# Kernel optimization log

Hardware: AMD Instinct MI355X
Metric: run time of the kernel (lower is better)

The kernel has to match this reference:

```python
import jax, jax.numpy as jnp
import numpy as np
from jax.scipy.linalg import solve_triangular

N, S, G, D = 2048, 64, 1, 512


def setup_inputs() -> dict:
    key = jax.random.key(0)
    k1, k2, k3, k4 = jax.random.split(key, 4)
    x = jax.random.normal(k1, (N, D), jnp.float32)
    mu = jax.random.uniform(k2, (S, G, D), jnp.float32) - 0.5  # torch.rand(...) - 0.5
    omega = jax.random.normal(k3, (S, G), jnp.float32)
    # original init sets sigma_p = eye; perturb so m = A^T A has distinct eigenvalues
    sigma_p = jnp.eye(D, dtype=jnp.float32)[None, None] + 0.05 * jax.random.normal(k4, (S, G, D, D), jnp.float32)
    return {"x": x, "mu": mu, "omega": omega, "sigma_p": sigma_p}


def reference(x, mu, omega, sigma_p):
    d = x.shape[-1]
    # m = sigma_p^T @ sigma_p  (symmetric PSD), per class/component
    m = jnp.einsum('sgki,sgkj->sgij', sigma_p, sigma_p)  # (S,G,D,D)
    # torch: sigma = m + 0.01 * diag_embed(eig(m).eigenvalues.real) * eye(d)
    # m is symmetric PSD -> eigenvalues are real; eigvalsh is the batched symmetric form
    eigvals = jnp.linalg.eigvalsh(m)  # (S,G,D)
    sigma = m + 0.01 * eigvals[..., None] * jnp.eye(d, dtype=m.dtype)  # adds diag(eigvals)
    _ = jax.nn.softmax(omega, -1)  # computed in original forward but unused in output
    mu0 = mu[:, 0]        # (S,D)   only component 0 is used
    sig0 = sigma[:, 0]    # (S,D,D)
    # MultivariateNormal.log_prob via Cholesky, batched over classes and samples
    L = jnp.linalg.cholesky(sig0)               # (S,D,D)
    diff = x[None, :, :] - mu0[:, None, :]      # (S,N,D)
    z = solve_triangular(L, diff.swapaxes(-1, -2), lower=True)  # (S,D,N)
    maha = jnp.sum(z * z, axis=1)               # (S,N)
    logdet = 2.0 * jnp.sum(jnp.log(jnp.diagonal(L, axis1=-2, axis2=-1)), axis=-1)  # (S,)
    logp = -0.5 * (maha + logdet[:, None] + d * jnp.log(jnp.asarray(2.0 * np.pi, m.dtype)))
    return logp.T  # (N,S)
```

## Files before the change

kernel.cpp:

```cpp
#include <hip/hip_runtime.h>

#define D 512
#define TW 16

__device__ __forceinline__ float waveSum(float v) {
#pragma unroll
    for (int m = 32; m > 0; m >>= 1) v += __shfl_xor(v, m, 64);
    return v;
}
__device__ __forceinline__ float waveMin(float v) {
#pragma unroll
    for (int m = 32; m > 0; m >>= 1) v = fminf(v, __shfl_xor(v, m, 64));
    return v;
}
__device__ __forceinline__ float waveMax(float v) {
#pragma unroll
    for (int m = 32; m > 0; m >>= 1) v = fmaxf(v, __shfl_xor(v, m, 64));
    return v;
}

__global__ __launch_bounds__(256) void xpose_kernel(const float* __restrict__ x,
                                                    float* __restrict__ xT) {
    __shared__ float t[64][65];
    const int bx = blockIdx.x * 64;
    const int by = blockIdx.y * 64;
    const int tid = threadIdx.x;
    const int lx = tid & 63, lq = tid >> 6;
#pragma unroll
    for (int r = 0; r < 64; r += 4)
        t[r + lq][lx] = x[(size_t)(bx + r + lq) * D + by + lx];
    __syncthreads();
#pragma unroll
    for (int r = 0; r < 64; r += 4)
        xT[(size_t)(by + r + lq) * 2048 + bx + lx] = t[lx][r + lq];
}

__global__ __launch_bounds__(256) void syrk_kernel(const float* __restrict__ sp,
                                                   float* __restrict__ M) {
    const int s = blockIdx.y;
    const int I = blockIdx.x >> 3, J = blockIdx.x & 7;
    const int tx = threadIdx.x & 15, ty = threadIdx.x >> 4;
    const float* __restrict__ A = sp + (size_t)s * D * D;
    __shared__ __align__(16) float As[64 * 68];
    __shared__ __align__(16) float Bs[64 * 68];
    float acc[4][4];
#pragma unroll
    for (int r = 0; r < 4; r++)
#pragma unroll
        for (int q = 0; q < 4; q++) acc[r][q] = 0.f;

    for (int k0 = 0; k0 < D; k0 += 64) {
        for (int e = threadIdx.x; e < 4096; e += 256) {
            const int col = e & 63, kr = e >> 6;
            As[kr * 68 + col] = A[(size_t)(k0 + kr) * D + I * 64 + col];
            Bs[kr * 68 + col] = A[(size_t)(k0 + kr) * D + J * 64 + col];
        }
        __syncthreads();
#pragma unroll 4
        for (int k = 0; k < 64; k++) {
            const float4 a = *(const float4*)&As[k * 68 + 4 * ty];
            const float4 b = *(const float4*)&Bs[k * 68 + 4 * tx];
            const float av[4] = {a.x, a.y, a.z, a.w};
            const float bv[4] = {b.x, b.y, b.z, b.w};
#pragma unroll
            for (int r = 0; r < 4; r++)
#pragma unroll
                for (int q = 0; q < 4; q++) acc[r][q] += av[r] * bv[q];
        }
        __syncthreads();
    }
#pragma unroll
    for (int r = 0; r < 4; r++) {
        float4 v4;
        v4.x = acc[r][0]; v4.y = acc[r][1]; v4.z = acc[r][2]; v4.w = acc[r][3];
        const size_t off = (size_t)s * D * D + (size_t)(I * 64 + 4 * ty + r) * D + J * 64 + 4 * tx;
        *(float4*)(M + off) = v4;
    }
}

__global__ __launch_bounds__(1024) void latrd_panel(float* __restrict__ T,
                                                    float* __restrict__ Vt,
                                                    float* __restrict__ Wt,
                                                    float* __restrict__ dvec,
                                                    float* __restrict__ evec,
                                                    int ps, int jmax) {
    const int s = blockIdx.x;
    float* __restrict__ Ts = T + (size_t)s * D * D;
    float* __restrict__ Vg = Vt + (size_t)s * 32 * D;
    float* __restrict__ Wg = Wt + (size_t)s * 32 * D;
    const int tid = threadIdx.x, lane = tid & 63, wid = tid >> 6;
    const int l4 = lane & 15, quad = lane >> 4;
    extern __shared__ float sm[];
    float* __restrict__ Vs = sm;
    float* __restrict__ Ws = sm + 16896;
    float* __restrict__ vb = sm + 33792;
    float* __restrict__ pf = sm + 34304;
    float* __restrict__ c1 = sm + 34816;
    float* __restrict__ c2 = sm + 34848;
    float* __restrict__ red = sm + 34880;
    float* __restrict__ sca = sm + 34896;

    for (int i = tid; i < 34304; i += 1024) sm[i] = 0.f;
    __syncthreads();

    float rk = (tid < D) ? Ts[(size_t)ps * D + tid] : 0.f;

    for (int j = 0; j < jmax; j++) {
        const int k = ps + j, sup = k + 1;
        float val = 0.f;
        if (tid < D && tid > k) {
            float corr = 0.f;
#pragma unroll 4
            for (int t = 0; t < j; t++)
                corr += Vs[tid * 33 + t] * Ws[k * 33 + t]
                      + Ws[tid * 33 + t] * Vs[k * 33 + t];
            val = rk - corr;
            vb[tid] = val;
            if (tid == sup) sca[3] = val;
        } else if (tid == k) {
            float dc = 0.f;
            for (int t = 0; t < j; t++) dc += Vs[k * 33 + t] * Ws[k * 33 + t];
            dvec[s * D + k] = rk - 2.f * dc;
            vb[k] = 0.f;
        }
        float xp = (tid < D && tid > sup) ? val * val : 0.f;
        xp = waveSum(xp);
        if (lane == 0) red[wid] = xp;
        __syncthreads();

        float xn2 = 0.f;
#pragma unroll
        for (int q = 0; q < TW; q++) xn2 += red[q];
        const float a0 = sca[3];
        const int skip = (xn2 <= 0.f);
        float beta = 0.f, v0 = 0.f, alpha = a0;
        if (!skip) {
            const float an = sqrtf(a0 * a0 + xn2);
            alpha = (a0 >= 0.f) ? -an : an;
            v0 = a0 - alpha;
            beta = 2.f / (v0 * v0 + xn2);
        }
        if (tid == sup) {
            evec[s * D + k] = skip ? a0 : alpha;
            if (!skip) vb[sup] = v0;
        }
        if (!skip) {
            const int t = tid >> 5, r = tid & 31;
            float a1 = 0.f, a2 = 0.f;
            for (int i = sup + 1 + r; i < D; i += 32) {
                const float v = vb[i];
                a1 += Ws[i * 33 + t] * v;
                a2 += Vs[i * 33 + t] * v;
            }
#pragma unroll
            for (int m = 16; m > 0; m >>= 1) {
                a1 += __shfl_xor(a1, m, 64);
                a2 += __shfl_xor(a2, m, 64);
            }
            if (r == 0) {
                c1[t] = a1 + Ws[sup * 33 + t] * v0;
                c2[t] = a2 + Vs[sup * 33 + t] * v0;
            }
        }
        __syncthreads();
        if (skip) {
            if (tid < D && tid >= sup) { Vg[j * D + tid] = 0.f; Wg[j * D + tid] = 0.f; }
            if (tid < D && k + 1 < D) rk = Ts[(size_t)(k + 1) * D + tid];
            __syncthreads();
            continue;
        }

        const int w0 = sup & ~63;
        float pvw = 0.f;
        for (int i = sup + (wid * 4 + quad); i < D; i += 64) {
            const float* __restrict__ row = Ts + (size_t)i * D;
            float4 a4 = {0.f, 0.f, 0.f, 0.f};
            for (int c = w0 + 4 * l4; c < D; c += 64) {
                const float4 a = *(const float4*)&row[c];
                const float4 b = *(const float4*)&vb[c];
                a4.x += a.x * b.x; a4.y += a.y * b.y;
                a4.z += a.z * b.z; a4.w += a.w * b.w;
            }
            float t1 = (a4.x + a4.y) + (a4.z + a4.w);
            t1 -= Vs[i * 33 + l4] * c1[l4] + Vs[i * 33 + l4 + 16] * c1[l4 + 16]
                + Ws[i * 33 + l4] * c2[l4] + Ws[i * 33 + l4 + 16] * c2[l4 + 16];
#pragma unroll
            for (int m = 1; m < 16; m <<= 1) t1 += __shfl_xor(t1, m, 64);
            const float p = beta * t1;
            if (l4 == 0) pf[i] = p;
            pvw += p * vb[i];
        }
        pvw += __shfl_xor(pvw, 16, 64);
        pvw += __shfl_xor(pvw, 32, 64);
        if (lane == 0) red[wid] = pvw;
        __syncthreads();

        float pv = 0.f;
#pragma unroll
        for (int q = 0; q < TW; q++) pv += red[q];
        const float cc = 0.5f * beta * pv;
        if (tid < D) {
            if (tid >= sup) {
                const float v = vb[tid];
                const float w = pf[tid] - cc * v;
                Vs[tid * 33 + j] = v;
                Ws[tid * 33 + j] = w;
                Vg[j * D + tid] = v;
                Wg[j * D + tid] = w;
            }
            if (k + 1 < D) rk = Ts[(size_t)(k + 1) * D + tid];
        }
        __syncthreads();
    }
    if (ps + jmax == D - 2 && tid == 0) {
        const int k1 = D - 2, k2 = D - 1;
        float dc = 0.f, ec = 0.f, dc2 = 0.f;
        for (int t = 0; t < jmax; t++) {
            dc  += Vs[k1 * 33 + t] * Ws[k1 * 33 + t];
            ec  += Vs[k1 * 33 + t] * Ws[k2 * 33 + t]
                 + Ws[k1 * 33 + t] * Vs[k2 * 33 + t];
            dc2 += Vs[k2 * 33 + t] * Ws[k2 * 33 + t];
        }
        dvec[s * D + k1] = Ts[(size_t)k1 * D + k1] - 2.f * dc;
        evec[s * D + k1] = Ts[(size_t)k1 * D + k2] - ec;
        dvec[s * D + k2] = Ts[(size_t)k2 * D + k2] - 2.f * dc2;
        evec[s * D + k2] = 0.f;
    }
}

__global__ __launch_bounds__(256) void latrd_update(float* __restrict__ T,
                                                    const float* __restrict__ Vt,
                                                    const float* __restrict__ Wt,
                                                    int r0) {
    const int s = blockIdx.z;
    const int i0 = r0 + 64 * blockIdx.y;
    const int j0 = r0 + 64 * blockIdx.x;
    float* __restrict__ Ts = T + (size_t)s * D * D;
    const float* __restrict__ Vg = Vt + (size_t)s * 32 * D;
    const float* __restrict__ Wg = Wt + (size_t)s * 32 * D;
    __shared__ __align__(16) float Vi[32 * 68], Wi[32 * 68], Vj[32 * 68], Wj[32 * 68];
    const int tid = threadIdx.x, tx = tid & 15, ty = tid >> 4;
    const float4 z4 = {0.f, 0.f, 0.f, 0.f};
    for (int e = tid; e < 512; e += 256) {
        const int t = e >> 4, c4 = (e & 15) * 4;
        const int gi = i0 + c4, gj = j0 + c4;
        *(float4*)&Vi[t * 68 + c4] = (gi < D) ? *(const float4*)&Vg[t * D + gi] : z4;
        *(float4*)&Wi[t * 68 + c4] = (gi < D) ? *(const float4*)&Wg[t * D + gi] : z4;
        *(float4*)&Vj[t * 68 + c4] = (gj < D) ? *(const float4*)&Vg[t * D + gj] : z4;
        *(float4*)&Wj[t * 68 + c4] = (gj < D) ? *(const float4*)&Wg[t * D + gj] : z4;
    }
    __syncthreads();
    float acc[4][4] = {{0.f}};
#pragma unroll 4
    for (int t = 0; t < 32; t++) {
        const float4 va = *(const float4*)&Vi[t * 68 + 4 * ty];
        const float4 wa = *(const float4*)&Wi[t * 68 + 4 * ty];
        const float4 vc = *(const float4*)&Vj[t * 68 + 4 * tx];
        const float4 wc = *(const float4*)&Wj[t * 68 + 4 * tx];
        const float av[4] = {va.x, va.y, va.z, va.w};
        const float aw[4] = {wa.x, wa.y, wa.z, wa.w};
        const float bv[4] = {vc.x, vc.y, vc.z, vc.w};
        const float bw[4] = {wc.x, wc.y, wc.z, wc.w};
#pragma unroll
        for (int r = 0; r < 4; r++)
#pragma unroll
            for (int q = 0; q < 4; q++) acc[r][q] += av[r] * bw[q] + aw[r] * bv[q];
    }
    const int gj = j0 + 4 * tx;
    if (gj >= D) return;
#pragma unroll
    for (int r = 0; r < 4; r++) {
        const int gi = i0 + 4 * ty + r;
        if (gi >= D) continue;
        float4 c = *(float4*)&Ts[(size_t)gi * D + gj];
        c.x -= acc[r][0]; c.y -= acc[r][1]; c.z -= acc[r][2]; c.w -= acc[r][3];
        *(float4*)&Ts[(size_t)gi * D + gj] = c;
    }
}

__global__ __launch_bounds__(512) void bisect_kernel(const float* __restrict__ dvec,
                                                     const float* __restrict__ evec,
                                                     float* __restrict__ lam) {
    const int s = blockIdx.x, tid = threadIdx.x;
    const int lane = tid & 63, wid = tid >> 6;
    __shared__ float d[D], e2[D], ea[D];
    __shared__ float red[8];
    __shared__ float sh_lo, sh_hi;
    {
        const float dv = dvec[s * D + tid];
        const float ev = evec[s * D + tid];
        d[tid] = dv; ea[tid] = fabsf(ev); e2[tid] = ev * ev;
    }
    __syncthreads();
    const float rad = ea[tid] + ((tid > 0) ? ea[tid - 1] : 0.f);
    float lo = waveMin(d[tid] - rad);
    float hi = waveMax(d[tid] + rad);
    if (lane == 0) red[wid] = lo;
    __syncthreads();
    if (tid == 0) {
        float t = red[0];
        for (int q = 1; q < 8; q++) t = fminf(t, red[q]);
        sh_lo = t - 1e-3f * fmaxf(fabsf(t), 1.f);
    }
    __syncthreads();
    if (lane == 0) red[wid] = hi;
    __syncthreads();
    if (tid == 0) {
        float t = red[0];
        for (int q = 1; q < 8; q++) t = fmaxf(t, red[q]);
        sh_hi = t + 1e-3f * fmaxf(fabsf(t), 1.f);
    }
    __syncthreads();
    float a = sh_lo, b = sh_hi;
    const int j1 = tid + 1;
    for (int it = 0; it < 36; it++) {
        const float mid = 0.5f * (a + b);
        int cnt = 0;
        float q = d[0] - mid;
        cnt += (q < 0.f);
        for (int i = 1; i < D; i++) {
            float den = q;
            const float ad = fabsf(den);
            den = (ad < 1e-26f) ? ((den < 0.f) ? -1e-26f : 1e-26f) : den;
            q = d[i] - mid - e2[i - 1] / den;
            cnt += (q < 0.f);
        }
        if (cnt >= j1) b = mid; else a = mid;
    }
    lam[s * D + tid] = 0.5f * (a + b);
}

__global__ __launch_bounds__(256) void chol_panel(float* __restrict__ M,
                                                  const float* __restrict__ lam,
                                                  float* __restrict__ logdet,
                                                  float* __restrict__ Lp,
                                                  int j0, int first) {
    const int s = blockIdx.x;
    float* __restrict__ Ms = M + (size_t)s * D * D;
    float* __restrict__ Lps = Lp + (size_t)s * 32 * D;
    const int tid = threadIdx.x, lane = tid & 63, wid = tid >> 6;
    extern __shared__ float smc[];
    float* __restrict__ P = smc;
    const int Wd = D - j0;
    for (int e = tid; e < 32 * D; e += 256) {
        const int t = e >> 9, i = e & 511;
        if (i >= j0) {
            const int il = i - j0;
            float v = Ms[(size_t)(j0 + t) * D + i];
            if (il == t) v += 0.01f * lam[s * D + j0 + t];
            P[t * 520 + il] = v;
        }
    }
    __syncthreads();
    float lacc = 0.f;
    for (int jl = 0; jl < 32; jl++) {
        const float pd = P[jl * 520 + jl];
        const float inv = 1.f / sqrtf(pd);
        if (tid == 0) { lacc += 0.5f * logf(pd); P[jl * 520 + jl] = sqrtf(pd); }
        for (int il = jl + 1 + tid; il < Wd; il += 256) P[jl * 520 + il] *= inv;
        __syncthreads();
        for (int kk = jl + 1 + wid; kk < 32; kk += 4) {
            const float f = P[jl * 520 + kk];
            for (int il = kk + lane; il < Wd; il += 64) P[kk * 520 + il] -= f * P[jl * 520 + il];
        }
        __syncthreads();
    }
    if (tid == 0) logdet[s] = (first ? 0.f : logdet[s]) + 2.f * lacc;
    for (int e = tid; e < 32 * D; e += 256) {
        const int t = e >> 9, i = e & 511;
        const int il = i - j0;
        if (il >= t) Ms[(size_t)(j0 + t) * D + i] = P[t * 520 + il];
        if (i >= j0 + 32) Lps[(size_t)t * D + i] = P[t * 520 + il];
    }
}

__global__ __launch_bounds__(256) void chol_update(float* __restrict__ M,
                                                   const float* __restrict__ Lp,
                                                   int r0) {
    if (blockIdx.x < blockIdx.y) return;
    const int s = blockIdx.z;
    const int i0 = r0 + 64 * blockIdx.y;
    const int j0 = r0 + 64 * blockIdx.x;
    float* __restrict__ Ms = M + (size_t)s * D * D;
    const float* __restrict__ Lps = Lp + (size_t)s * 32 * D;
    __shared__ __align__(16) float Li[32 * 68], Lj[32 * 68];
    const int tid = threadIdx.x, tx = tid & 15, ty = tid >> 4;
    const float4 z4 = {0.f, 0.f, 0.f, 0.f};
    for (int e = tid; e < 512; e += 256) {
        const int t = e >> 4, c4 = (e & 15) * 4;
        const int gi = i0 + c4, gj = j0 + c4;
        *(float4*)&Li[t * 68 + c4] = (gi < D) ? *(const float4*)&Lps[(size_t)t * D + gi] : z4;
        *(float4*)&Lj[t * 68 + c4] = (gj < D) ? *(const float4*)&Lps[(size_t)t * D + gj] : z4;
    }
    __syncthreads();
    float acc[4][4] = {{0.f}};
#pragma unroll 4
    for (int t = 0; t < 32; t++) {
        const float4 a = *(const float4*)&Li[t * 68 + 4 * ty];
        const float4 b = *(const float4*)&Lj[t * 68 + 4 * tx];
        const float av[4] = {a.x, a.y, a.z, a.w};
        const float bv[4] = {b.x, b.y, b.z, b.w};
#pragma unroll
        for (int r = 0; r < 4; r++)
#pragma unroll
            for (int q = 0; q < 4; q++) acc[r][q] += av[r] * bv[q];
    }
    const int gj = j0 + 4 * tx;
    if (gj >= D) return;
#pragma unroll
    for (int r = 0; r < 4; r++) {
        const int gi = i0 + 4 * ty + r;
        if (gi >= D) continue;
        float4 c = *(float4*)&Ms[(size_t)gi * D + gj];
        c.x -= acc[r][0]; c.y -= acc[r][1]; c.z -= acc[r][2]; c.w -= acc[r][3];
        *(float4*)&Ms[(size_t)gi * D + gj] = c;
    }
}

__global__ __launch_bounds__(64) void invdiag_kernel(const float* __restrict__ M,
                                                     float* __restrict__ invDT) {
    const int b = blockIdx.x, s = b >> 3, I = b & 7;
    const int c = threadIdx.x;
    __shared__ float Lsh[64 * 65];
    __shared__ float xsh[64 * 65];
    const float* __restrict__ Ms = M + (size_t)s * D * D;
    for (int e = c; e < 4096; e += 64) {
        const int i = e & 63, k = e >> 6;
        Lsh[i * 65 + k] = Ms[(size_t)(I * 64 + k) * D + I * 64 + i];
    }
    for (int i = 0; i < 64; i++) xsh[c * 65 + i] = (i == c) ? 1.f : 0.f;
    __syncthreads();
    for (int i = 0; i < 64; i++) {
        float t = xsh[c * 65 + i];
        for (int k = 0; k < i; k++) t -= Lsh[i * 65 + k] * xsh[c * 65 + k];
        xsh[c * 65 + i] = t / Lsh[i * 65 + i];
    }
    float* __restrict__ outp = invDT + (size_t)b * 4096 + c * 64;
    for (int i = 0; i < 64; i++) outp[i] = xsh[c * 65 + i];
}

__global__ __launch_bounds__(256) void triinv_step(float* __restrict__ M,
                                                   const float* __restrict__ invDT,
                                                   int I) {
    const int J = blockIdx.x, s = blockIdx.y;
    float* __restrict__ Ms = M + (size_t)s * D * D;
    __shared__ __align__(16) float Ls[64 * 68];
    __shared__ __align__(16) float Bs[64 * 68];
    __shared__ __align__(16) float Ss[64 * 68];
    const int tid = threadIdx.x, tx = tid & 15, ty = tid >> 4;
    float acc[4][4] = {{0.f}};
    for (int K = J; K < I; K++) {
        __syncthreads();
        for (int e = tid; e < 4096; e += 256) {
            const int k = e >> 6, r = e & 63;
            Ls[k * 68 + r] = Ms[(size_t)(K * 64 + k) * D + I * 64 + r];
        }
        if (K == J) {
            const float* __restrict__ dJ = invDT + ((size_t)s * 8 + J) * 4096;
            for (int e = tid; e < 4096; e += 256) {
                const int c = e >> 6, k = e & 63;
                Bs[k * 68 + c] = dJ[c * 64 + k];
            }
        } else {
            for (int e = tid; e < 4096; e += 256) {
                const int k = e >> 6, c = e & 63;
                Bs[k * 68 + c] = Ms[(size_t)(K * 64 + k) * D + J * 64 + c];
            }
        }
        __syncthreads();
#pragma unroll 4
        for (int k = 0; k < 64; k++) {
            const float4 a = *(const float4*)&Ls[k * 68 + 4 * ty];
            const float4 b = *(const float4*)&Bs[k * 68 + 4 * tx];
            const float av[4] = {a.x, a.y, a.z, a.w};
            const float bv[4] = {b.x, b.y, b.z, b.w};
#pragma unroll
            for (int r = 0; r < 4; r++)
#pragma unroll
                for (int q = 0; q < 4; q++) acc[r][q] += av[r] * bv[q];
        }
    }
    __syncthreads();
#pragma unroll
    for (int r = 0; r < 4; r++) {
        float4 v4;
        v4.x = acc[r][0]; v4.y = acc[r][1]; v4.z = acc[r][2]; v4.w = acc[r][3];
        *(float4*)&Ss[(4 * ty + r) * 68 + 4 * tx] = v4;
    }
    {
        const float* __restrict__ dI = invDT + ((size_t)s * 8 + I) * 4096;
        for (int e = tid; e < 4096; e += 256) {
            const int k = e >> 6, r = e & 63;
            Ls[k * 68 + r] = dI[k * 64 + r];
        }
    }
    __syncthreads();
    float o[4][4] = {{0.f}};
#pragma unroll 4
    for (int k = 0; k < 64; k++) {
        const float4 a = *(const float4*)&Ls[k * 68 + 4 * ty];
        const float4 b = *(const float4*)&Ss[k * 68 + 4 * tx];
        const float av[4] = {a.x, a.y, a.z, a.w};
        const float bv[4] = {b.x, b.y, b.z, b.w};
#pragma unroll
        for (int r = 0; r < 4; r++)
#pragma unroll
            for (int q = 0; q < 4; q++) o[r][q] += av[r] * bv[q];
    }
#pragma unroll
    for (int r = 0; r < 4; r++) {
        float4 v4;
        v4.x = -o[r][0]; v4.y = -o[r][1]; v4.z = -o[r][2]; v4.w = -o[r][3];
        *(float4*)&Ms[(size_t)(I * 64 + 4 * ty + r) * D + J * 64 + 4 * tx] = v4;
    }
}

__global__ __launch_bounds__(256) void gemm_maha(const float* __restrict__ M,
                                                 const float* __restrict__ invDT,
                                                 const float* __restrict__ xT,
                                                 const float* __restrict__ mu,
                                                 const float* __restrict__ logdet,
                                                 float* __restrict__ out) {
    const int s = blockIdx.y;
    const int n0 = blockIdx.x * 64;
    const int tid = threadIdx.x, tx = tid & 15, ty = tid >> 4;
    const float* __restrict__ Ms = M + (size_t)s * D * D;
    const float* __restrict__ mus = mu + s * D;
    __shared__ __align__(16) float As[32 * 136];
    __shared__ __align__(16) float Bs[32 * 68];
    __shared__ float red[16 * 68];
    float cs[4] = {0.f, 0.f, 0.f, 0.f};

    for (int ci = 0; ci < 4; ci++) {
        const int i0 = ci * 128;
        float acc[8][4];
#pragma unroll
        for (int r = 0; r < 8; r++)
#pragma unroll
            for (int q = 0; q < 4; q++) acc[r][q] = 0.f;
        const int nkc = (ci + 1) * 4;
        for (int kc = 0; kc < nkc; kc++) {
            const int k0 = kc * 32, kb = k0 >> 6;
            __syncthreads();
            for (int e = tid; e < 4096; e += 256) {
                const int il = e >> 5, kk = e & 31;
                const int ib = (i0 + il) >> 6;
                As[kk * 136 + il] = (kb < ib) ? Ms[(size_t)(i0 + il) * D + k0 + kk] : 0.f;
            }
            if (kb >= 2 * ci) {
                const float* __restrict__ dB = invDT + ((size_t)s * 8 + kb) * 4096
                                             + (size_t)(k0 & 63) * 64;
                const int ilb = (kb - 2 * ci) * 64;
                for (int e = tid; e < 2048; e += 256) {
                    const int ii = e & 63, kk = e >> 6;
                    As[kk * 136 + ilb + ii] = dB[kk * 64 + ii];
                }
            }
            for (int e = tid; e < 2048; e += 256) {
                const int nn = e & 63, kk = e >> 6;
                Bs[kk * 68 + nn] = xT[(size_t)(k0 + kk) * 2048 + n0 + nn] - mus[k0 + kk];
            }
            __syncthreads();
#pragma unroll 8
            for (int kk = 0; kk < 32; kk++) {
                const float4 a0 = *(const float4*)&As[kk * 136 + 8 * ty];
                const float4 a1 = *(const float4*)&As[kk * 136 + 8 * ty + 4];
                const float4 b  = *(const float4*)&Bs[kk * 68 + 4 * tx];
                const float av[8] = {a0.x, a0.y, a0.z, a0.w, a1.x, a1.y, a1.z, a1.w};
                const float bv[4] = {b.x, b.y, b.z, b.w};
#pragma unroll
                for (int r = 0; r < 8; r++)
#pragma unroll
                    for (int q = 0; q < 4; q++) acc[r][q] += av[r] * bv[q];
            }
        }
#pragma unroll
        for (int r = 0; r < 8; r++)
#pragma unroll
            for (int q = 0; q < 4; q++) cs[q] += acc[r][q] * acc[r][q];
    }
    __syncthreads();
#pragma unroll
    for (int q = 0; q < 4; q++) red[ty * 68 + 4 * tx + q] = cs[q];
    __syncthreads();
    if (tid < 64) {
        float mah = 0.f;
#pragma unroll
        for (int t = 0; t < 16; t++) mah += red[t * 68 + tid];
        out[(size_t)(n0 + tid) * 64 + s] = -0.5f * (mah + logdet[s] + 940.993058f);
    }
}

extern "C" void kernel_launch(void* const* d_in, const int* in_sizes, int n_in,
                              void* d_out, int out_size, void* d_ws, size_t ws_size,
                              hipStream_t stream) {
    const float* x  = (const float*)d_in[0];
    const float* mu = (const float*)d_in[1];
    const float* sp = (const float*)d_in[3];
    float* out = (float*)d_out;

    float* wsf  = (float*)d_ws;
    float* MT   = wsf;
    float* dvec = wsf + (size_t)16777216;
    float* evec = dvec + 32768;
    float* lamv = evec + 32768;
    float* logd = lamv + 32768;
    float* Vt   = logd + 64;
    float* Wt   = Vt + (size_t)1048576;
    float* xT   = Wt + (size_t)1048576;
    float* Lp   = Vt;
    float* invDT = Vt;

    xpose_kernel<<<dim3(32, 8), dim3(256), 0, stream>>>(x, xT);
    syrk_kernel<<<dim3(64, 64), dim3(256), 0, stream>>>(sp, MT);

    const size_t plds = (size_t)34900 * sizeof(float);
    for (int p = 0; p < 16; p++) {
        const int ps = 32 * p;
        const int jmax = (p == 15) ? 30 : 32;
        latrd_panel<<<dim3(64), dim3(1024), plds, stream>>>(MT, Vt, Wt, dvec, evec, ps, jmax);
        if (p < 15) {
            const int r0 = ps + 32;
            const int nt = (D - r0 + 63) / 64;
            latrd_update<<<dim3(nt, nt, 64), dim3(256), 0, stream>>>(MT, Vt, Wt, r0);
        }
    }

    bisect_kernel<<<dim3(64), dim3(512), 0, stream>>>(dvec, evec, lamv);

    syrk_kernel<<<dim3(64, 64), dim3(256), 0, stream>>>(sp, MT);
    const size_t clds = (size_t)(32 * 520 + 4) * sizeof(float);
    for (int p = 0; p < 16; p++) {
        const int j0 = 32 * p;
        chol_panel<<<dim3(64), dim3(256), clds, stream>>>(MT, lamv, logd, Lp, j0, p == 0 ? 1 : 0);
        if (p < 15) {
            const int r0 = j0 + 32;
            const int nt = (D - r0 + 63) / 64;
            chol_update<<<dim3(nt, nt, 64), dim3(256), 0, stream>>>(MT, Lp, r0);
        }
    }

    invdiag_kernel<<<dim3(512), dim3(64), 0, stream>>>(MT, invDT);
    for (int I = 1; I < 8; I++)
        triinv_step<<<dim3(I, 64), dim3(256), 0, stream>>>(MT, invDT, I);

    gemm_maha<<<dim3(32, 64), dim3(256), 0, stream>>>(MT, invDT, xT, mu, logd, out);
}
```

Measured before the change: 11.14 ms.

## Exploit symmetry in LATRD matvec and split bisection across more blocks

The symmetric matrix-vector product in the tridiagonalization panel now walks only the lower-triangle 64x64 tiles. Each off-diagonal tile is used twice, once for the row product and once transposed, with results accumulated in shared memory through atomics. This roughly halves global reads of the trailing matrix, at the cost of shared-memory atomics and a separate pass for the low-rank correction. The eigenvalue bisection kernel is split into 4 blocks per matrix to spread work across more CUs. It also drops from 36 to 26 iterations and uses a hardware reciprocal instead of a guarded divide, which trades accuracy for speed.

```diff
diff --git a/kernel.cpp b/kernel.cpp
--- a/kernel.cpp
+++ b/kernel.cpp
@@ -108,6 +108,7 @@
     for (int j = 0; j < jmax; j++) {
         const int k = ps + j, sup = k + 1;
         float val = 0.f;
+        if (tid < D) pf[tid] = 0.f;
         if (tid < D && tid > k) {
             float corr = 0.f;
 #pragma unroll 4
@@ -170,29 +171,51 @@
             continue;
         }
 
-        const int w0 = sup & ~63;
-        float pvw = 0.f;
-        for (int i = sup + (wid * 4 + quad); i < D; i += 64) {
-            const float* __restrict__ row = Ts + (size_t)i * D;
-            float4 a4 = {0.f, 0.f, 0.f, 0.f};
-            for (int c = w0 + 4 * l4; c < D; c += 64) {
-                const float4 a = *(const float4*)&row[c];
-                const float4 b = *(const float4*)&vb[c];
-                a4.x += a.x * b.x; a4.y += a.y * b.y;
-                a4.z += a.z * b.z; a4.w += a.w * b.w;
-            }
-            float t1 = (a4.x + a4.y) + (a4.z + a4.w);
-            t1 -= Vs[i * 33 + l4] * c1[l4] + Vs[i * 33 + l4 + 16] * c1[l4 + 16]
-                + Ws[i * 33 + l4] * c2[l4] + Ws[i * 33 + l4 + 16] * c2[l4 + 16];
-#pragma unroll
-            for (int m = 1; m < 16; m <<= 1) t1 += __shfl_xor(t1, m, 64);
-            const float p = beta * t1;
-            if (l4 == 0) pf[i] = p;
-            pvw += p * vb[i];
-        }
-        pvw += __shfl_xor(pvw, 16, 64);
-        pvw += __shfl_xor(pvw, 32, 64);
-        if (lane == 0) red[wid] = pvw;
+        {
+            const int b0 = sup >> 6, tb = 8 - b0, ntile = tb * (tb + 1) / 2;
+            for (int tt = wid; tt < ntile; tt += TW) {
+                int ri = 0, acc0 = 0;
+                while (acc0 + ri + 1 <= tt) { acc0 += ri + 1; ri++; }
+                const int cj = tt - acc0;
+                const int gi0 = (b0 + ri) << 6, gj0 = (b0 + cj) << 6;
+                for (int rr = quad; rr < 64; rr += 4) {
+                    const float4 a = *(const float4*)&Ts[(size_t)(gi0 + rr) * D + gj0 + 4 * l4];
+                    const float4 b = *(const float4*)&vb[gj0 + 4 * l4];
+                    float sum = a.x * b.x + a.y * b.y + a.z * b.z + a.w * b.w;
+                    sum += __shfl_xor(sum, 1, 64);
+                    sum += __shfl_xor(sum, 2, 64);
+                    sum += __shfl_xor(sum, 4, 64);
+                    sum += __shfl_xor(sum, 8, 64);
+                    if (l4 == 0) atomicAdd(&pf[gi0 + rr], sum);
+                }
+                if (ri != cj) {
+                    const float* __restrict__ base = Ts + (size_t)gi0 * D + gj0 + lane;
+                    float y0 = 0.f, y1 = 0.f, y2 = 0.f, y3 = 0.f;
+#pragma unroll 4
+                    for (int rr = 0; rr < 64; rr += 4) {
+                        y0 += base[(size_t)(rr    ) * D] * vb[gi0 + rr];
+                        y1 += base[(size_t)(rr + 1) * D] * vb[gi0 + rr + 1];
+                        y2 += base[(size_t)(rr + 2) * D] * vb[gi0 + rr + 2];
+                        y3 += base[(size_t)(rr + 3) * D] * vb[gi0 + rr + 3];
+                    }
+                    atomicAdd(&pf[gj0 + lane], (y0 + y1) + (y2 + y3));
+                }
+            }
+        }
+        __syncthreads();
+
+        float pvp = 0.f;
+        if (tid < D && tid >= sup) {
+            float corr = 0.f;
+#pragma unroll 8
+            for (int t = 0; t < 32; t++)
+                corr += Vs[tid * 33 + t] * c1[t] + Ws[tid * 33 + t] * c2[t];
+            const float p = beta * (pf[tid] - corr);
+            pf[tid] = p;
+            pvp = p * vb[tid];
+        }
+        pvp = waveSum(pvp);
+        if (lane == 0) red[wid] = pvp;
         __syncthreads();
 
         float pv = 0.f;
@@ -278,56 +301,46 @@
     }
 }
 
-__global__ __launch_bounds__(512) void bisect_kernel(const float* __restrict__ dvec,
+__global__ __launch_bounds__(128) void bisect_kernel(const float* __restrict__ dvec,
                                                      const float* __restrict__ evec,
                                                      float* __restrict__ lam) {
-    const int s = blockIdx.x, tid = threadIdx.x;
-    const int lane = tid & 63, wid = tid >> 6;
-    __shared__ float d[D], e2[D], ea[D];
-    __shared__ float red[8];
-    __shared__ float sh_lo, sh_hi;
-    {
-        const float dv = dvec[s * D + tid];
-        const float ev = evec[s * D + tid];
-        d[tid] = dv; ea[tid] = fabsf(ev); e2[tid] = ev * ev;
-    }
-    __syncthreads();
-    const float rad = ea[tid] + ((tid > 0) ? ea[tid - 1] : 0.f);
-    float lo = waveMin(d[tid] - rad);
-    float hi = waveMax(d[tid] + rad);
-    if (lane == 0) red[wid] = lo;
-    __syncthreads();
-    if (tid == 0) {
-        float t = red[0];
-        for (int q = 1; q < 8; q++) t = fminf(t, red[q]);
-        sh_lo = t - 1e-3f * fmaxf(fabsf(t), 1.f);
-    }
-    __syncthreads();
-    if (lane == 0) red[wid] = hi;
-    __syncthreads();
-    if (tid == 0) {
-        float t = red[0];
-        for (int q = 1; q < 8; q++) t = fmaxf(t, red[q]);
-        sh_hi = t + 1e-3f * fmaxf(fabsf(t), 1.f);
-    }
-    __syncthreads();
-    float a = sh_lo, b = sh_hi;
-    const int j1 = tid + 1;
-    for (int it = 0; it < 36; it++) {
+    const int s = blockIdx.y, seg = blockIdx.x;
+    const int tid = threadIdx.x;
+    __shared__ float d[D], e2c[D], ea[D];
+    __shared__ float rlo[2], rhi[2];
+    for (int i = tid; i < D; i += 128) {
+        d[i] = dvec[s * D + i];
+        const float ev = evec[s * D + i];
+        ea[i] = fabsf(ev);
+        e2c[i] = fmaxf(ev * ev, 1e-34f);
+    }
+    __syncthreads();
+    float lo = 1e30f, hi = -1e30f;
+    for (int i = tid; i < D; i += 128) {
+        const float rad = ea[i] + ((i > 0) ? ea[i - 1] : 0.f);
+        lo = fminf(lo, d[i] - rad);
+        hi = fmaxf(hi, d[i] + rad);
+    }
+    lo = waveMin(lo); hi = waveMax(hi);
+    if ((tid & 63) == 0) { rlo[tid >> 6] = lo; rhi[tid >> 6] = hi; }
+    __syncthreads();
+    lo = fminf(rlo[0], rlo[1]); hi = fmaxf(rhi[0], rhi[1]);
+    lo -= 1e-3f * fmaxf(fabsf(lo), 1.f);
+    hi += 1e-3f * fmaxf(fabsf(hi), 1.f);
+    float a = lo, b = hi;
+    const int j1 = seg * 128 + tid + 1;
+    for (int it = 0; it < 26; it++) {
         const float mid = 0.5f * (a + b);
         int cnt = 0;
         float q = d[0] - mid;
         cnt += (q < 0.f);
         for (int i = 1; i < D; i++) {
-            float den = q;
-            const float ad = fabsf(den);
-            den = (ad < 1e-26f) ? ((den < 0.f) ? -1e-26f : 1e-26f) : den;
-            q = d[i] - mid - e2[i - 1] / den;
+            q = d[i] - mid - e2c[i - 1] * __builtin_amdgcn_rcpf(q);
             cnt += (q < 0.f);
         }
         if (cnt >= j1) b = mid; else a = mid;
     }
-    lam[s * D + tid] = 0.5f * (a + b);
+    lam[s * D + seg * 128 + tid] = 0.5f * (a + b);
 }
 
 __global__ __launch_bounds__(256) void chol_panel(float* __restrict__ M,
@@ -626,7 +639,7 @@
         }
     }
 
-    bisect_kernel<<<dim3(64), dim3(512), 0, stream>>>(dvec, evec, lamv);
+    bisect_kernel<<<dim3(4, 64), dim3(128), 0, stream>>>(dvec, evec, lamv);
 
     syrk_kernel<<<dim3(64, 64), dim3(256), 0, stream>>>(sp, MT);
     const size_t clds = (size_t)(32 * 520 + 4) * sizeof(float);
```

After: 12.09 ms. 8.5% more time.
